# Kernel optimization log

Hardware: AMD Instinct MI355X
Metric: run time of the kernel (lower is better)

## Reference

```python
import jax, jax.numpy as jnp
import numpy as np

H = 16  # num_attention_heads

def setup_inputs() -> dict:
    key = jax.random.key(0)
    ks = jax.random.split(key, 4)
    B, S, D = 4, 2048, 1024
    scale = 1.0 / np.sqrt(D)
    return {
        "hidden_states": jax.random.normal(ks[0], (B, S, D), dtype=jnp.float32),
        "attention_mask": jnp.zeros((B, 1, 1, S), dtype=jnp.float32),
        "Wq": jax.random.normal(ks[1], (D, D), dtype=jnp.float32) * scale,
        "bq": jnp.zeros((D,), dtype=jnp.float32),
        "Wk": jax.random.normal(ks[2], (D, D), dtype=jnp.float32) * scale,
        "bk": jnp.zeros((D,), dtype=jnp.float32),
        "Wv": jax.random.normal(ks[3], (D, D), dtype=jnp.float32) * scale,
        "bv": jnp.zeros((D,), dtype=jnp.float32),
    }

def _split_heads(x, B, S):
    # [B,S,D] -> [B,H,S,Dh]
    return x.reshape(B, S, H, -1).transpose(0, 2, 1, 3)

def reference(hidden_states, attention_mask, Wq, bq, Wk, bk, Wv, bv):
    B, S, D = hidden_states.shape
    Dh = D // H
    q = _split_heads(hidden_states @ Wq.T + bq, B, S)  # [B,H,S,Dh]
    k = _split_heads(hidden_states @ Wk.T + bk, B, S)
    v = _split_heads(hidden_states @ Wv.T + bv, B, S)
    scores = jnp.einsum("bhqd,bhkd->bhqk", q, k) / jnp.sqrt(jnp.float32(Dh))
    scores = scores + attention_mask  # additive mask, broadcast [B,1,1,S]
    probs = jax.nn.softmax(scores, axis=-1)  # dropout is identity in eval mode
    ctx = jnp.einsum("bhqk,bhkd->bhqd", probs, v)  # [B,H,S,Dh]
    ctx = ctx.transpose(0, 2, 1, 3).reshape(B, S, D)
    return ctx
```

## Files before the change

### kernel.cpp

```cpp
#include <hip/hip_runtime.h>
#include <hip/hip_bf16.h>
#include <stdint.h>

#define LOG2E 1.44269504088896340736f
#define SCL   (0.125f * LOG2E)

typedef __attribute__((ext_vector_type(8)))  short short8;
typedef __attribute__((ext_vector_type(16))) float floatx16;
typedef __attribute__((ext_vector_type(4)))  unsigned short ushort4v;

#define GLP(g, l)                                                              \
    __builtin_amdgcn_global_load_lds(                                          \
        (const __attribute__((address_space(1))) void*)(g),                    \
        (__attribute__((address_space(3))) void*)(l), 16, 0, 0)

#if __has_builtin(__builtin_amdgcn_exp2f)
#define EXP2(x) __builtin_amdgcn_exp2f(x)
#else
#define EXP2(x) exp2f(x)
#endif

static __device__ __forceinline__ unsigned short f2bf(float f) {
    union { float f; unsigned u; } v; v.f = f;
    unsigned r = v.u + 0x7FFFu + ((v.u >> 16) & 1u);
    return (unsigned short)(r >> 16);
}

static __device__ __forceinline__ unsigned pack2bf(float a, float b) {
    __hip_bfloat162 h = __float22bfloat162_rn(make_float2(a, b));
    union { __hip_bfloat162 h; unsigned u; } c; c.h = h; return c.u;
}

__global__ __launch_bounds__(256) void cvt_kernel(const float* __restrict__ in,
                                                  unsigned short* __restrict__ out,
                                                  int n4) {
    int i = blockIdx.x * 256 + threadIdx.x;
    if (i < n4) {
        float4 v = ((const float4*)in)[i];
        ushort4v o;
        o.x = f2bf(v.x); o.y = f2bf(v.y); o.z = f2bf(v.z); o.w = f2bf(v.w);
        ((ushort4v*)out)[i] = o;
    }
}

__global__ __launch_bounds__(256) void cvt_w3m(const float* __restrict__ Wq,
                                               const float* __restrict__ Wk,
                                               const float* __restrict__ Wv,
                                               const float* __restrict__ mask,
                                               unsigned short* __restrict__ out,
                                               float* __restrict__ maskl) {
    int i = blockIdx.x * 256 + threadIdx.x;
    if (i < 786432) {
        const float* src; int j;
        if (i < 262144)      { src = Wq; j = i; }
        else if (i < 524288) { src = Wk; j = i - 262144; }
        else                 { src = Wv; j = i - 524288; }
        float4 v = ((const float4*)src)[j];
        ushort4v o;
        o.x = f2bf(v.x); o.y = f2bf(v.y); o.z = f2bf(v.z); o.w = f2bf(v.w);
        ((ushort4v*)out)[i] = o;
    } else if (i < 786432 + 2048) {
        int j = i - 786432;
        float4 v = ((const float4*)mask)[j];
        ((float4*)maskl)[j] = make_float4(v.x * LOG2E, v.y * LOG2E,
                                          v.z * LOG2E, v.w * LOG2E);
    }
}

__global__ __launch_bounds__(256) void qkv_gemm(
        const unsigned short* __restrict__ X,
        const unsigned short* __restrict__ W,
        const float* __restrict__ bq, const float* __restrict__ bk,
        const float* __restrict__ bv,
        unsigned short* __restrict__ Qf,
        unsigned short* __restrict__ Kf,
        unsigned short* __restrict__ Vt)
{
    __shared__ __align__(16) unsigned short sh[17408];
    unsigned short* Ash = sh;
    unsigned short* Bsh = sh + 8192;

    const int tid  = threadIdx.x;
    const int lane = tid & 63;
    const int wv   = tid >> 6;
    const int q32  = lane & 31;
    const int hi   = lane >> 5;
    const int mBase = blockIdx.x * 128;
    const int nBase = blockIdx.y * 128;
    const int wm = (wv >> 1) * 64;
    const int wn = (wv & 1) * 64;

    floatx16 acc[2][2];
    acc[0][0] = 0.0f; acc[0][1] = 0.0f; acc[1][0] = 0.0f; acc[1][1] = 0.0f;

    const int sr = lane >> 3;
    const int kc = (lane & 7) ^ sr;

    for (int kb = 0; kb < 1024; kb += 64) {
        __syncthreads();
#pragma unroll
        for (int s = 0; s < 4; ++s) {
            const int seg = wv * 4 + s;
            const int row = seg * 8 + sr;
            GLP(X + (size_t)(mBase + row) * 1024 + kb + kc * 8, Ash + seg * 512);
            GLP(W + (size_t)(nBase + row) * 1024 + kb + kc * 8, Bsh + seg * 512);
        }
        __syncthreads();
#pragma unroll
        for (int ks = 0; ks < 4; ++ks) {
            short8 aF[2], bF[2];
#pragma unroll
            for (int mi = 0; mi < 2; ++mi) {
                const int R = wm + mi * 32 + q32;
                const int slot = (2 * ks + hi) ^ (R & 7);
                aF[mi] = *(const short8*)(Ash + (R >> 3) * 512 + (R & 7) * 64 + slot * 8);
            }
#pragma unroll
            for (int ni = 0; ni < 2; ++ni) {
                const int R = wn + ni * 32 + q32;
                const int slot = (2 * ks + hi) ^ (R & 7);
                bF[ni] = *(const short8*)(Bsh + (R >> 3) * 512 + (R & 7) * 64 + slot * 8);
            }
#pragma unroll
            for (int mi = 0; mi < 2; ++mi)
#pragma unroll
                for (int ni = 0; ni < 2; ++ni)
                    acc[mi][ni] = __builtin_amdgcn_mfma_f32_32x32x16_bf16(
                        aF[mi], bF[ni], acc[mi][ni], 0, 0, 0);
        }
    }

    if (blockIdx.y < 16) {
        unsigned short* dst = (blockIdx.y < 8) ? Qf : Kf;
        const float* bias   = (blockIdx.y < 8) ? bq : bk;
        const float scl     = (blockIdx.y < 8) ? SCL : 1.0f;
        const int nb = nBase & 1023;
        float bj[2];
#pragma unroll
        for (int ni = 0; ni < 2; ++ni)
            bj[ni] = bias[nb + wn + ni * 32 + q32];
        __syncthreads();
#pragma unroll
        for (int ni = 0; ni < 2; ++ni) {
            const int col = wn + ni * 32 + q32;
#pragma unroll
            for (int mi = 0; mi < 2; ++mi)
#pragma unroll
                for (int g = 0; g < 4; ++g) {
                    const int row0 = wm + mi * 32 + g * 8 + hi * 4;
#pragma unroll
                    for (int rr = 0; rr < 4; ++rr)
                        sh[(row0 + rr) * 136 + col] =
                            f2bf((acc[mi][ni][g * 4 + rr] + bj[ni]) * scl);
                }
        }
        __syncthreads();
#pragma unroll
        for (int it = 0; it < 8; ++it) {
            const int row  = it * 16 + (tid >> 4);
            const int part = tid & 15;
            short8 v = *(const short8*)(sh + row * 136 + part * 8);
            *(short8*)(dst + (size_t)(mBase + row) * 1024 + nb + part * 8) = v;
        }
    } else {
#pragma unroll
        for (int ni = 0; ni < 2; ++ni) {
            const int gn = nBase + wn + ni * 32 + q32;
            const int c  = gn & 1023;
            const int h  = c >> 6;
            const int d  = c & 63;
            const float bias = bv[c];
#pragma unroll
            for (int mi = 0; mi < 2; ++mi)
#pragma unroll
                for (int g = 0; g < 4; ++g) {
                    const int m0 = mBase + wm + mi * 32 + g * 8 + hi * 4;
                    const int b  = m0 >> 11;
                    const int s0 = m0 & 2047;
                    ushort4v pv;
#pragma unroll
                    for (int rr = 0; rr < 4; ++rr)
                        pv[rr] = f2bf(acc[mi][ni][g * 4 + rr] + bias);
                    *(ushort4v*)(Vt + (size_t)((b * 16 + h) * 64 + d) * 2048 + s0) = pv;
                }
        }
    }
}

__global__ __launch_bounds__(256, 4) void attn_kernel(
        const unsigned short* __restrict__ Qf,
        const unsigned short* __restrict__ Kf,
        const unsigned short* __restrict__ VT,
        const float* __restrict__ maskl,
        float* __restrict__ out)
{
    __shared__ __align__(16) unsigned short Ksh[128 * 64];
    __shared__ __align__(16) unsigned short Vsh[64 * 128];
    __shared__ __align__(16) float Msh[128];
    __shared__ __align__(16) float Lsh[128];

    const int tid  = threadIdx.x;
    const int lane = tid & 63;
    const int wv   = tid >> 6;
    const int q32  = lane & 31;
    const int hi   = lane >> 5;
    const int bh   = blockIdx.x & 63;
    const int qt   = blockIdx.x >> 6;
    const int b    = bh >> 4;
    const int h    = bh & 15;
    const int q0   = qt * 128 + wv * 32;
    const int sw   = q32 & 7;

    short8 bQ[4];
#pragma unroll
    for (int ks = 0; ks < 4; ++ks)
        bQ[ks] = *(const short8*)(Qf + (size_t)(b * 2048 + q0 + q32) * 1024
                                     + h * 64 + ks * 16 + hi * 8);

    floatx16 accO0 = 0.0f, accO1 = 0.0f;
    float l_c = 0.0f;

    const unsigned short* gK = Kf + (size_t)(b * 2048) * 1024 + h * 64;
    const unsigned short* gV = VT + (size_t)(bh * 64) * 2048;
    const float* mrow = maskl + b * 2048;

    const unsigned short* kb4[4];
    const unsigned short* vb4[4];
#pragma unroll
    for (int ks = 0; ks < 4; ++ks) {
        const int cs = (2 * ks + hi) ^ sw;
        kb4[ks] = Ksh + q32 * 64 + cs * 8;
        vb4[ks] = Vsh + q32 * 128 + cs * 8;
    }
    const float* mbase = Msh + hi * 4;

    const int krr = lane >> 3;
    const int kcs = lane & 7;
    const int vrr = lane >> 4;
    const int vcs = lane & 15;

    for (int kb = 0; kb < 2048; kb += 128) {
        __syncthreads();
#pragma unroll
        for (int s = 0; s < 4; ++s) {
            const int seg = wv * 4 + s;
            const int rK  = seg * 8 + krr;
            const int cK  = kcs ^ (rK & 7);
            GLP(gK + (size_t)(kb + rK) * 1024 + cK * 8, Ksh + seg * 512);
            const int rV  = seg * 4 + vrr;
            const int cV  = vcs ^ (rV & 7);
            GLP(gV + (size_t)rV * 2048 + kb + cV * 8, Vsh + seg * 512);
        }
        if (tid < 32) GLP(mrow + kb + lane * 4, Msh);
        __syncthreads();

#pragma unroll
        for (int half = 0; half < 2; ++half) {
#pragma unroll
            for (int mt = 0; mt < 2; ++mt) {
                floatx16 sacc;
#pragma unroll
                for (int a = 0; a < 4; ++a) {
                    float4 mv4 = *(const float4*)(mbase + half * 64 + mt * 32 + a * 8);
                    sacc[a * 4 + 0] = mv4.x; sacc[a * 4 + 1] = mv4.y;
                    sacc[a * 4 + 2] = mv4.z; sacc[a * 4 + 3] = mv4.w;
                }
#pragma unroll
                for (int ks = 0; ks < 4; ++ks) {
                    short8 aK = *(const short8*)(kb4[ks] + half * 4096 + mt * 2048);
                    sacc = __builtin_amdgcn_mfma_f32_32x32x16_bf16(aK, bQ[ks], sacc, 0, 0, 0);
                }
                unsigned u0[4], u1[4], e0[4], e1[4];
#pragma unroll
                for (int a = 0; a < 4; ++a) {
                    float p0 = EXP2(sacc[a * 4 + 0]);
                    float p1 = EXP2(sacc[a * 4 + 1]);
                    float p2 = EXP2(sacc[a * 4 + 2]);
                    float p3 = EXP2(sacc[a * 4 + 3]);
                    l_c += (p0 + p1) + (p2 + p3);
                    u0[a] = pack2bf(p0, p1);
                    u1[a] = pack2bf(p2, p3);
                    e0[a] = (unsigned)__shfl_xor((int)u0[a], 32, 64);
                    e1[a] = (unsigned)__shfl_xor((int)u1[a], 32, 64);
                }
#pragma unroll
                for (int ks2 = 0; ks2 < 2; ++ks2) {
                    const int a0 = ks2 * 2;
                    union { unsigned u[4]; short8 s; } aP;
                    aP.u[0] = hi ? e0[a0 + 1] : u0[a0];
                    aP.u[1] = hi ? e1[a0 + 1] : u1[a0];
                    aP.u[2] = hi ? u0[a0 + 1] : e0[a0];
                    aP.u[3] = hi ? u1[a0 + 1] : e1[a0];
                    const int ks = mt * 2 + ks2;
                    short8 bV0 = *(const short8*)(vb4[ks] + half * 64);
                    short8 bV1 = *(const short8*)(vb4[ks] + 4096 + half * 64);
                    accO0 = __builtin_amdgcn_mfma_f32_32x32x16_bf16(aP.s, bV0, accO0, 0, 0, 0);
                    accO1 = __builtin_amdgcn_mfma_f32_32x32x16_bf16(aP.s, bV1, accO1, 0, 0, 0);
                }
            }
        }
    }

    l_c += __shfl_xor(l_c, 32, 64);
    if (lane < 32) Lsh[wv * 32 + q32] = 1.0f / l_c;
#pragma unroll
    for (int g = 0; g < 4; ++g) {
        float4 inv4 = *(const float4*)(Lsh + wv * 32 + g * 8 + hi * 4);
#pragma unroll
        for (int rr = 0; rr < 4; ++rr) {
            const int r   = g * 4 + rr;
            const int row = rr + 8 * g + 4 * hi;
            const float linv = (rr == 0) ? inv4.x : (rr == 1) ? inv4.y
                             : (rr == 2) ? inv4.z : inv4.w;
            float* op = out + (size_t)(b * 2048 + q0 + row) * 1024 + h * 64 + q32;
            op[0]  = accO0[r] * linv;
            op[32] = accO1[r] * linv;
        }
    }
}

extern "C" void kernel_launch(void* const* d_in, const int* in_sizes, int n_in,
                              void* d_out, int out_size, void* d_ws, size_t ws_size,
                              hipStream_t stream) {
    const float* X    = (const float*)d_in[0];
    const float* mask = (const float*)d_in[1];
    const float* Wq   = (const float*)d_in[2];
    const float* bq   = (const float*)d_in[3];
    const float* Wk   = (const float*)d_in[4];
    const float* bk   = (const float*)d_in[5];
    const float* Wv   = (const float*)d_in[6];
    const float* bv   = (const float*)d_in[7];
    float* out = (float*)d_out;

    char* ws = (char*)d_ws;
    unsigned short* xb  = (unsigned short*)(ws);
    unsigned short* wb  = (unsigned short*)(ws + 16777216);
    unsigned short* qf  = (unsigned short*)(ws + 23068672);
    unsigned short* kf  = (unsigned short*)(ws + 39845888);
    unsigned short* vtb = (unsigned short*)(ws + 56623104);
    float*          ml  = (float*)(ws + 73400320);

    cvt_kernel<<<8192, 256, 0, stream>>>(X, xb, 2097152);
    cvt_w3m<<<3080, 256, 0, stream>>>(Wq, Wk, Wv, mask, wb, ml);

    qkv_gemm<<<dim3(64, 24), 256, 0, stream>>>(xb, wb, bq, bk, bv, qf, kf, vtb);

    attn_kernel<<<1024, 256, 0, stream>>>(qf, kf, vtb, ml, out);
}
```

Measured before the change: 262.2 us.

## Permute V^T key order to drop P shuffles and merge conversion kernels

The QKV GEMM now stores V-transposed with bits 2 and 3 of the sequence index swapped. This permuted key order matches the MFMA accumulator layout of the probability tile, so the attention kernel can feed the packed bf16 probabilities straight in as the A operand. That removes the cross-lane __shfl_xor exchanges and selects per tile. Separately, the X conversion and the weight/mask conversion kernels are merged into one launch to save a kernel launch. The approach relies on the permutation matching the K-side key ordering exactly.

```diff
diff --git a/kernel.cpp b/kernel.cpp
--- a/kernel.cpp
+++ b/kernel.cpp
@@ -31,36 +31,32 @@
     union { __hip_bfloat162 h; unsigned u; } c; c.h = h; return c.u;
 }
 
-__global__ __launch_bounds__(256) void cvt_kernel(const float* __restrict__ in,
-                                                  unsigned short* __restrict__ out,
-                                                  int n4) {
-    int i = blockIdx.x * 256 + threadIdx.x;
-    if (i < n4) {
-        float4 v = ((const float4*)in)[i];
-        ushort4v o;
-        o.x = f2bf(v.x); o.y = f2bf(v.y); o.z = f2bf(v.z); o.w = f2bf(v.w);
-        ((ushort4v*)out)[i] = o;
-    }
-}
-
-__global__ __launch_bounds__(256) void cvt_w3m(const float* __restrict__ Wq,
+__global__ __launch_bounds__(256) void cvt_all(const float* __restrict__ X,
+                                               const float* __restrict__ Wq,
                                                const float* __restrict__ Wk,
                                                const float* __restrict__ Wv,
                                                const float* __restrict__ mask,
-                                               unsigned short* __restrict__ out,
+                                               unsigned short* __restrict__ xb,
+                                               unsigned short* __restrict__ wb,
                                                float* __restrict__ maskl) {
     int i = blockIdx.x * 256 + threadIdx.x;
-    if (i < 786432) {
-        const float* src; int j;
-        if (i < 262144)      { src = Wq; j = i; }
-        else if (i < 524288) { src = Wk; j = i - 262144; }
-        else                 { src = Wv; j = i - 524288; }
-        float4 v = ((const float4*)src)[j];
+    if (i < 2097152) {
+        float4 v = ((const float4*)X)[i];
         ushort4v o;
         o.x = f2bf(v.x); o.y = f2bf(v.y); o.z = f2bf(v.z); o.w = f2bf(v.w);
-        ((ushort4v*)out)[i] = o;
-    } else if (i < 786432 + 2048) {
-        int j = i - 786432;
+        ((ushort4v*)xb)[i] = o;
+    } else if (i < 2883584) {
+        int j = i - 2097152;
+        const float* src; int k;
+        if (j < 262144)      { src = Wq; k = j; }
+        else if (j < 524288) { src = Wk; k = j - 262144; }
+        else                 { src = Wv; k = j - 524288; }
+        float4 v = ((const float4*)src)[k];
+        ushort4v o;
+        o.x = f2bf(v.x); o.y = f2bf(v.y); o.z = f2bf(v.z); o.w = f2bf(v.w);
+        ((ushort4v*)wb)[j] = o;
+    } else if (i < 2883584 + 2048) {
+        int j = i - 2883584;
         float4 v = ((const float4*)mask)[j];
         ((float4*)maskl)[j] = make_float4(v.x * LOG2E, v.y * LOG2E,
                                           v.z * LOG2E, v.w * LOG2E);
@@ -177,11 +173,12 @@
                     const int m0 = mBase + wm + mi * 32 + g * 8 + hi * 4;
                     const int b  = m0 >> 11;
                     const int s0 = m0 & 2047;
+                    const int sp = (s0 & ~12) | ((s0 & 4) << 1) | ((s0 & 8) >> 1);
                     ushort4v pv;
 #pragma unroll
                     for (int rr = 0; rr < 4; ++rr)
                         pv[rr] = f2bf(acc[mi][ni][g * 4 + rr] + bias);
-                    *(ushort4v*)(Vt + (size_t)((b * 16 + h) * 64 + d) * 2048 + s0) = pv;
+                    *(ushort4v*)(Vt + (size_t)((b * 16 + h) * 64 + d) * 2048 + sp) = pv;
                 }
         }
     }
@@ -270,7 +267,7 @@
                     short8 aK = *(const short8*)(kb4[ks] + half * 4096 + mt * 2048);
                     sacc = __builtin_amdgcn_mfma_f32_32x32x16_bf16(aK, bQ[ks], sacc, 0, 0, 0);
                 }
-                unsigned u0[4], u1[4], e0[4], e1[4];
+                unsigned u[8];
 #pragma unroll
                 for (int a = 0; a < 4; ++a) {
                     float p0 = EXP2(sacc[a * 4 + 0]);
@@ -278,19 +275,16 @@
                     float p2 = EXP2(sacc[a * 4 + 2]);
                     float p3 = EXP2(sacc[a * 4 + 3]);
                     l_c += (p0 + p1) + (p2 + p3);
-                    u0[a] = pack2bf(p0, p1);
-                    u1[a] = pack2bf(p2, p3);
-                    e0[a] = (unsigned)__shfl_xor((int)u0[a], 32, 64);
-                    e1[a] = (unsigned)__shfl_xor((int)u1[a], 32, 64);
+                    u[2 * a]     = pack2bf(p0, p1);
+                    u[2 * a + 1] = pack2bf(p2, p3);
                 }
 #pragma unroll
                 for (int ks2 = 0; ks2 < 2; ++ks2) {
-                    const int a0 = ks2 * 2;
-                    union { unsigned u[4]; short8 s; } aP;
-                    aP.u[0] = hi ? e0[a0 + 1] : u0[a0];
-                    aP.u[1] = hi ? e1[a0 + 1] : u1[a0];
-                    aP.u[2] = hi ? u0[a0 + 1] : e0[a0];
-                    aP.u[3] = hi ? u1[a0 + 1] : e1[a0];
+                    union { unsigned uu[4]; short8 s; } aP;
+                    aP.uu[0] = u[4 * ks2 + 0];
+                    aP.uu[1] = u[4 * ks2 + 1];
+                    aP.uu[2] = u[4 * ks2 + 2];
+                    aP.uu[3] = u[4 * ks2 + 3];
                     const int ks = mt * 2 + ks2;
                     short8 bV0 = *(const short8*)(vb4[ks] + half * 64);
                     short8 bV1 = *(const short8*)(vb4[ks] + 4096 + half * 64);
@@ -340,8 +334,7 @@
     unsigned short* vtb = (unsigned short*)(ws + 56623104);
     float*          ml  = (float*)(ws + 73400320);
 
-    cvt_kernel<<<8192, 256, 0, stream>>>(X, xb, 2097152);
-    cvt_w3m<<<3080, 256, 0, stream>>>(Wq, Wk, Wv, mask, wb, ml);
+    cvt_all<<<11272, 256, 0, stream>>>(X, Wq, Wk, Wv, mask, xb, wb, ml);
 
     qkv_gemm<<<dim3(64, 24), 256, 0, stream>>>(xb, wb, bq, bk, bv, qf, kf, vtb);
 
```

After: 243.7 us. 7.1% less time.
